# Kernel optimization log

Measured on AMD Instinct MI355X. Metric: run time of the kernel, lower is better.

The kernel has to match this reference:

```python
import jax, jax.numpy as jnp
import numpy as np

NUM_EXPERTS = 8
IN_FEATURES = 2048
OUT_FEATURES = 5632
GROUP_SIZE = 64
NUM_TOKENS = 4096


def setup_inputs() -> dict:
    key = jax.random.key(0)
    k1, k2, k3, k4 = jax.random.split(key, 4)
    inp = jax.random.normal(k1, (NUM_TOKENS, IN_FEATURES), dtype=jnp.float32)
    # tokens are pre-sorted contiguously per expert; balanced routing
    tokens_per_expert = jnp.full((NUM_EXPERTS,), NUM_TOKENS // NUM_EXPERTS, dtype=jnp.int32)
    # int4 quantized weights stored as integer codes in [0, 16)
    weights = jax.random.randint(k2, (NUM_EXPERTS, IN_FEATURES, OUT_FEATURES), 0, 16, dtype=jnp.int32)
    n_groups = IN_FEATURES // GROUP_SIZE
    scales = jax.random.uniform(k3, (NUM_EXPERTS, n_groups, OUT_FEATURES, 1), dtype=jnp.float32,
                                minval=0.005, maxval=0.02)
    zeros = jax.random.normal(k4, (NUM_EXPERTS, n_groups, OUT_FEATURES, 1), dtype=jnp.float32) * 0.01
    scales_and_zeros = jnp.concatenate([scales, zeros], axis=-1)  # [E, K//G, N, 2]
    return {"input": inp, "tokens_per_expert": tokens_per_expert,
            "weights": weights, "scales_and_zeros": scales_and_zeros}


def _dequant(weights, scales_and_zeros):
    # torchao int4 convention: w = (q - 8) * scale + zero, grouped along K
    E, K, N = weights.shape
    n_groups = scales_and_zeros.shape[1]
    g = K // n_groups
    q = weights.astype(jnp.float32).reshape(E, n_groups, g, N)
    s = scales_and_zeros[..., 0][:, :, None, :]  # [E, K//G, 1, N]
    z = scales_and_zeros[..., 1][:, :, None, :]
    return ((q - 8.0) * s + z).reshape(E, K, N)


def reference(input, tokens_per_expert, weights, scales_and_zeros):
    num_tokens, K = input.shape
    E = weights.shape[0]
    W = _dequant(weights, scales_and_zeros)  # [E, K, N] float32
    # expert id of each (contiguous-sorted) token from cumsum boundaries
    cum = jnp.cumsum(tokens_per_expert)                      # [E]
    seg = jnp.searchsorted(cum, jnp.arange(num_tokens), side='right')  # [T]
    start = jnp.concatenate([jnp.zeros((1,), cum.dtype), cum[:-1]])
    pos = jnp.arange(num_tokens) - start[seg]                # slot within expert block
    # capacity-based grouped GEMM (balanced routing in setup: C = T // E)
    C = num_tokens // E
    buf = jnp.zeros((E, C, K), input.dtype).at[seg, pos].set(input)
    y = jnp.einsum('eck,ekn->ecn', buf, W)                   # per-expert GEMM
    return y[seg, pos]                                       # [T, N]
```

## Files before the change

### kernel.cpp

```cpp
#include <hip/hip_runtime.h>

#define NE    8
#define KDIM  2048
#define NDIM  5632
#define NTOK  4096
#define CAP   512
#define NGRP  32
#define BM    128
#define BN    128
#define BK    32
#define MT    4
#define NT    44
#define LDSS  40

#define K8      (KDIM / 8)
#define NBLK_N  (NDIM / 256)
#define PACK_BLOCKS (NE * K8 * NBLK_N)
#define ACV_BLOCKS  (NTOK * KDIM / (8 * 256))
#define PACKED_BYTES ((size_t)NE * K8 * NDIM * 4)
#define ABF_BYTES    ((size_t)NTOK * KDIM * 2)
#define WBT_BYTES    ((size_t)NE * NDIM * KDIM * 2)

#define KB_DQ (KDIM / 64)
#define NB_DQ (NDIM / 256)
#define DQT_BLOCKS (NE * KB_DQ * NB_DQ)

typedef __attribute__((ext_vector_type(8))) short bf16x8;
typedef __attribute__((ext_vector_type(4))) short bf16x4;
typedef __attribute__((ext_vector_type(4))) float f32x4;

static __device__ __forceinline__ short f2bf(float f) {
    union { float f; unsigned u; } x; x.f = f;
    unsigned r = (x.u + 0x7fffu + ((x.u >> 16) & 1u)) >> 16;
    return (short)r;
}

static __device__ __forceinline__ void gl2lds16(const unsigned short* g, short* l) {
    __builtin_amdgcn_global_load_lds(
        (const __attribute__((address_space(1))) unsigned int*)g,
        (__attribute__((address_space(3))) unsigned int*)l, 16, 0, 0);
}

__global__ __launch_bounds__(256)
void dq_kernel(const int* __restrict__ wq, const float* __restrict__ sz,
               const float* __restrict__ inp,
               unsigned short* __restrict__ wbt, unsigned short* __restrict__ abf)
{
    const int bid = blockIdx.x;
    if (bid < DQT_BLOCKS) {
        const int e  = bid / (KB_DQ * NB_DQ);
        const int r  = bid % (KB_DQ * NB_DQ);
        const int kb = r / NB_DQ;
        const int nb = r % NB_DQ;
        const int n  = nb * 256 + threadIdx.x;

        const int* src = wq + ((size_t)e * KDIM + kb * 64) * NDIM + n;
        const float2 s2 = *(const float2*)(sz + (((size_t)e * NGRP + kb) * NDIM + n) * 2);
        const float s  = s2.x;
        const float z8 = s2.y - 8.f * s2.x;
        unsigned short* dst = wbt + ((size_t)e * NDIM + n) * KDIM + kb * 64;

        #pragma unroll
        for (int o = 0; o < 8; ++o) {
            bf16x8 h;
            #pragma unroll
            for (int j = 0; j < 8; ++j) {
                const float q = (float)src[(size_t)(o * 8 + j) * NDIM];
                h[j] = f2bf(fmaf(q, s, z8));
            }
            *(bf16x8*)(dst + o * 8) = h;
        }
    } else {
        const size_t t = (size_t)(bid - DQT_BLOCKS) * 256 + threadIdx.x;
        const float4* p = (const float4*)inp + t * 2;
        const float4 v0 = p[0], v1 = p[1];
        bf16x8 h;
        h[0] = f2bf(v0.x); h[1] = f2bf(v0.y); h[2] = f2bf(v0.z); h[3] = f2bf(v0.w);
        h[4] = f2bf(v1.x); h[5] = f2bf(v1.y); h[6] = f2bf(v1.z); h[7] = f2bf(v1.w);
        *((bf16x8*)abf + t) = h;
    }
}

__global__ __launch_bounds__(256)
void hqq_gemm3(const unsigned short* __restrict__ abf,
               const unsigned short* __restrict__ wbt,
               float* __restrict__ out)
{
    const int bid = blockIdx.x;
    const int e   = bid & 7;
    const int rem = bid >> 3;
    const int nt  = rem >> 2;
    const int mt  = rem & 3;

    __shared__ __align__(16) short Alds[BM * BK];
    __shared__ __align__(16) short Blds[BN * BK];

    const int tid = threadIdx.x;
    const int m0  = e * CAP + mt * BM;
    const int n0  = nt * BN;

    const unsigned short* Ab = abf + (size_t)m0 * KDIM;
    const unsigned short* Bb = wbt + ((size_t)e * NDIM + n0) * KDIM;

    f32x4 acc[4][4];
    #pragma unroll
    for (int i = 0; i < 4; ++i)
        #pragma unroll
        for (int j = 0; j < 4; ++j)
            acc[i][j] = (f32x4){0.f, 0.f, 0.f, 0.f};

    const int wave = tid >> 6;
    const int lane = tid & 63;
    const int wm = (wave >> 1) << 6;
    const int wn = (wave & 1) << 6;
    const int lr = lane & 15;
    const int lq = lane >> 4;

    for (int k0 = 0; k0 < KDIM; k0 += BK) {
        #pragma unroll
        for (int p = 0; p < 2; ++p) {
            const int idx = p * 256 + tid;
            const int row = idx >> 2;
            const int kq  = idx & 3;
            gl2lds16(Ab + (size_t)row * KDIM + k0 + kq * 8, &Alds[idx * 8]);
            gl2lds16(Bb + (size_t)row * KDIM + k0 + kq * 8, &Blds[idx * 8]);
        }
        __syncthreads();

        bf16x8 af[4], bv[4];
        #pragma unroll
        for (int i = 0; i < 4; ++i)
            af[i] = *(const bf16x8*)&Alds[(wm + i * 16 + lr) * BK + lq * 8];
        #pragma unroll
        for (int j = 0; j < 4; ++j)
            bv[j] = *(const bf16x8*)&Blds[(wn + j * 16 + lr) * BK + lq * 8];
        #pragma unroll
        for (int i = 0; i < 4; ++i)
            #pragma unroll
            for (int j = 0; j < 4; ++j)
                acc[i][j] = __builtin_amdgcn_mfma_f32_16x16x32_bf16(af[i], bv[j], acc[i][j], 0, 0, 0);

        __syncthreads();
    }

    const int orow0 = m0 + wm + lq * 4;
    const int ocol0 = n0 + wn + lr;
    #pragma unroll
    for (int i = 0; i < 4; ++i)
        #pragma unroll
        for (int r = 0; r < 4; ++r) {
            float* op = out + (size_t)(orow0 + i * 16 + r) * NDIM + ocol0;
            #pragma unroll
            for (int j = 0; j < 4; ++j)
                op[j * 16] = acc[i][j][r];
        }
}

__global__ __launch_bounds__(256)
void pack_kernel(const int* __restrict__ wq, const float* __restrict__ inp,
                 unsigned* __restrict__ pw, unsigned short* __restrict__ abf)
{
    const int bid = blockIdx.x;
    if (bid < PACK_BLOCKS) {
        const int e  = bid / (K8 * NBLK_N);
        const int r  = bid % (K8 * NBLK_N);
        const int k8 = r / NBLK_N;
        const int nb = r % NBLK_N;
        const int n  = nb * 256 + threadIdx.x;
        const int* src = wq + ((size_t)e * KDIM + k8 * 8) * NDIM + n;
        unsigned v = 0;
        #pragma unroll
        for (int j = 0; j < 8; ++j)
            v |= (unsigned)(src[(size_t)j * NDIM] & 15) << (4 * j);
        pw[((size_t)e * K8 + k8) * NDIM + n] = v;
    } else {
        const size_t t = (size_t)(bid - PACK_BLOCKS) * 256 + threadIdx.x;
        const float4* p = (const float4*)inp + t * 2;
        const float4 v0 = p[0], v1 = p[1];
        bf16x8 h;
        h[0] = f2bf(v0.x); h[1] = f2bf(v0.y); h[2] = f2bf(v0.z); h[3] = f2bf(v0.w);
        h[4] = f2bf(v1.x); h[5] = f2bf(v1.y); h[6] = f2bf(v1.z); h[7] = f2bf(v1.w);
        *((bf16x8*)abf + t) = h;
    }
}

__global__ __launch_bounds__(256, 2)
void hqq_gemm2(const unsigned short* __restrict__ abf,
               const unsigned*       __restrict__ pw,
               const float*          __restrict__ sz,
               float*                __restrict__ out)
{
    const int bid = blockIdx.x;
    const int e   = bid / (MT * NT);
    const int rem = bid % (MT * NT);
    const int nt  = rem >> 2;
    const int mt  = rem & 3;

    __shared__ __align__(16) short Alds[BM * LDSS];
    __shared__ __align__(16) short Blds[BN * LDSS];

    const int tid = threadIdx.x;
    const int m0  = e * CAP + mt * BM;
    const int n0  = nt * BN;

    const int a_kq  = tid & 3;
    const int a_row = tid >> 2;
    const int b_n   = tid & 127;
    const int b_h   = tid >> 7;

    const unsigned short* Ab = abf + (size_t)m0 * KDIM;
    const unsigned*       Wb = pw  + (size_t)e * K8 * NDIM + n0 + b_n;
    const float*          SZb = sz + (size_t)e * NGRP * (NDIM * 2) + (size_t)(n0 + b_n) * 2;

    f32x4 acc[4][4];
    #pragma unroll
    for (int i = 0; i < 4; ++i)
        #pragma unroll
        for (int j = 0; j < 4; ++j)
            acc[i][j] = (f32x4){0.f, 0.f, 0.f, 0.f};

    const int wave = tid >> 6;
    const int lane = tid & 63;
    const int wm = (wave >> 1) << 6;
    const int wn = (wave & 1) << 6;
    const int lr = lane & 15;
    const int lq = lane >> 4;

    for (int k0 = 0; k0 < KDIM; k0 += BK) {
        const int g = k0 >> 6;
        #pragma unroll
        for (int p = 0; p < 2; ++p) {
            const int row = a_row + p * 64;
            const bf16x8 v = *(const bf16x8*)(Ab + (size_t)row * KDIM + k0 + a_kq * 8);
            *(bf16x8*)&Alds[row * LDSS + a_kq * 8] = v;
        }
        const float2 s2 = *(const float2*)(SZb + (size_t)g * (NDIM * 2));
        const float s  = s2.x;
        const float z8 = s2.y - 8.f * s2.x;
        const unsigned* wp = Wb + ((size_t)(k0 >> 3) + b_h * 2) * NDIM;
        const unsigned u0 = wp[0];
        const unsigned u1 = wp[NDIM];
        bf16x8 bb0, bb1;
        #pragma unroll
        for (int j = 0; j < 8; ++j) {
            bb0[j] = f2bf(fmaf((float)((u0 >> (4 * j)) & 15u), s, z8));
            bb1[j] = f2bf(fmaf((float)((u1 >> (4 * j)) & 15u), s, z8));
        }
        *(bf16x8*)&Blds[b_n * LDSS + b_h * 16]     = bb0;
        *(bf16x8*)&Blds[b_n * LDSS + b_h * 16 + 8] = bb1;

        __syncthreads();

        bf16x8 af[4], bfv[4];
        #pragma unroll
        for (int i = 0; i < 4; ++i)
            af[i] = *(const bf16x8*)&Alds[(wm + i * 16 + lr) * LDSS + lq * 8];
        #pragma unroll
        for (int j = 0; j < 4; ++j)
            bfv[j] = *(const bf16x8*)&Blds[(wn + j * 16 + lr) * LDSS + lq * 8];
        #pragma unroll
        for (int i = 0; i < 4; ++i)
            #pragma unroll
            for (int j = 0; j < 4; ++j)
                acc[i][j] = __builtin_amdgcn_mfma_f32_16x16x32_bf16(af[i], bfv[j], acc[i][j], 0, 0, 0);

        __syncthreads();
    }

    const int orow0 = m0 + wm + lq * 4;
    const int ocol0 = n0 + wn + lr;
    #pragma unroll
    for (int i = 0; i < 4; ++i)
        #pragma unroll
        for (int r = 0; r < 4; ++r) {
            float* op = out + (size_t)(orow0 + i * 16 + r) * NDIM + ocol0;
            #pragma unroll
            for (int j = 0; j < 4; ++j)
                op[j * 16] = acc[i][j][r];
        }
}

__global__ __launch_bounds__(256, 2)
void hqq_gemm_fallback(const float* __restrict__ inp,
                       const int*   __restrict__ wq,
                       const float* __restrict__ sz,
                       float*       __restrict__ out)
{
    const int bid = blockIdx.x;
    const int e   = bid / (MT * NT);
    const int rem = bid % (MT * NT);
    const int nt  = rem >> 2;
    const int mt  = rem & 3;

    __shared__ __align__(16) short Alds[BM * LDSS];
    __shared__ __align__(16) short Blds[BN * LDSS];

    const int tid = threadIdx.x;
    const int m0  = e * CAP + mt * BM;
    const int n0  = nt * BN;

    const int a_kq  = tid & 7;
    const int a_row = tid >> 3;
    const int b_n   = tid & 127;
    const int b_h   = tid >> 7;

    const float* Ab  = inp + (size_t)m0 * KDIM;
    const int*   Wb  = wq  + (size_t)e * KDIM * NDIM + n0 + b_n;
    const float* SZb = sz  + (size_t)e * NGRP * (NDIM * 2) + (size_t)(n0 + b_n) * 2;

    f32x4 acc[4][4];
    #pragma unroll
    for (int i = 0; i < 4; ++i)
        #pragma unroll
        for (int j = 0; j < 4; ++j)
            acc[i][j] = (f32x4){0.f, 0.f, 0.f, 0.f};

    const int wave = tid >> 6;
    const int lane = tid & 63;
    const int wm = (wave >> 1) << 6;
    const int wn = (wave & 1) << 6;
    const int lr = lane & 15;
    const int lq = lane >> 4;

    for (int k0 = 0; k0 < KDIM; k0 += BK) {
        const int g = k0 >> 6;
        #pragma unroll
        for (int p = 0; p < 4; ++p) {
            const int row = a_row + p * 32;
            const float4 v = *(const float4*)(Ab + (size_t)row * KDIM + k0 + a_kq * 4);
            bf16x4 h;
            h[0] = f2bf(v.x); h[1] = f2bf(v.y); h[2] = f2bf(v.z); h[3] = f2bf(v.w);
            *(bf16x4*)&Alds[row * LDSS + a_kq * 4] = h;
        }
        const float2 s2 = *(const float2*)(SZb + (size_t)g * (NDIM * 2));
        const float s  = s2.x;
        const float z8 = s2.y - 8.f * s2.x;
        #pragma unroll
        for (int oo = 0; oo < 2; ++oo) {
            const int ko = b_h * 8 + oo * 16;
            const int* wp = Wb + (size_t)(k0 + ko) * NDIM;
            bf16x8 bb;
            #pragma unroll
            for (int j = 0; j < 8; ++j) {
                const float q = (float)wp[(size_t)j * NDIM];
                bb[j] = f2bf(fmaf(q, s, z8));
            }
            *(bf16x8*)&Blds[b_n * LDSS + ko] = bb;
        }
        __syncthreads();
        bf16x8 af[4], bfv[4];
        #pragma unroll
        for (int i = 0; i < 4; ++i)
            af[i] = *(const bf16x8*)&Alds[(wm + i * 16 + lr) * LDSS + lq * 8];
        #pragma unroll
        for (int j = 0; j < 4; ++j)
            bfv[j] = *(const bf16x8*)&Blds[(wn + j * 16 + lr) * LDSS + lq * 8];
        #pragma unroll
        for (int i = 0; i < 4; ++i)
            #pragma unroll
            for (int j = 0; j < 4; ++j)
                acc[i][j] = __builtin_amdgcn_mfma_f32_16x16x32_bf16(af[i], bfv[j], acc[i][j], 0, 0, 0);
        __syncthreads();
    }

    const int orow0 = m0 + wm + lq * 4;
    const int ocol0 = n0 + wn + lr;
    #pragma unroll
    for (int i = 0; i < 4; ++i)
        #pragma unroll
        for (int r = 0; r < 4; ++r) {
            float* op = out + (size_t)(orow0 + i * 16 + r) * NDIM + ocol0;
            #pragma unroll
            for (int j = 0; j < 4; ++j)
                op[j * 16] = acc[i][j][r];
        }
}

extern "C" void kernel_launch(void* const* d_in, const int* in_sizes, int n_in,
                              void* d_out, int out_size, void* d_ws, size_t ws_size,
                              hipStream_t stream) {
    const float* inp = (const float*)d_in[0];
    const int*   wq  = (const int*)d_in[2];
    const float* sz  = (const float*)d_in[3];
    float*       out = (float*)d_out;

    if (ws_size >= ABF_BYTES + WBT_BYTES) {
        unsigned short* abf = (unsigned short*)d_ws;
        unsigned short* wbt = (unsigned short*)((char*)d_ws + ABF_BYTES);
        dq_kernel<<<dim3(DQT_BLOCKS + ACV_BLOCKS), dim3(256), 0, stream>>>(wq, sz, inp, wbt, abf);
        hqq_gemm3<<<dim3(NE * MT * NT), dim3(256), 0, stream>>>(abf, wbt, out);
    } else if (ws_size >= PACKED_BYTES + ABF_BYTES) {
        unsigned*       pw  = (unsigned*)d_ws;
        unsigned short* abf = (unsigned short*)((char*)d_ws + PACKED_BYTES);
        pack_kernel<<<dim3(PACK_BLOCKS + ACV_BLOCKS), dim3(256), 0, stream>>>(wq, inp, pw, abf);
        hqq_gemm2<<<dim3(NE * MT * NT), dim3(256), 0, stream>>>(abf, pw, sz, out);
    } else {
        hqq_gemm_fallback<<<dim3(NE * MT * NT), dim3(256), 0, stream>>>(inp, wq, sz, out);
    }
}
```

Baseline: 831.7 us.

## Transpose dequantized weights through swizzled LDS tiles for coalesced loads and stores

Each dequant-transpose block now handles a 128x128 (K,N) tile. It reads int32 codes with vectorized int4 loads, writes bf16 values into an XOR-swizzled shared-memory tile, and after a barrier writes contiguous 16-byte chunks along K into the transposed weight buffer. Before this, each thread walked a strided column and stored 16 bytes per row, which gave poorly coalesced global writes. In exchange the change uses 32 KB of LDS per block and adds a barrier, which can reduce occupancy for this pre-pass.

```diff
diff --git a/kernel.cpp b/kernel.cpp
--- a/kernel.cpp
+++ b/kernel.cpp
@@ -21,9 +21,9 @@
 #define ABF_BYTES    ((size_t)NTOK * KDIM * 2)
 #define WBT_BYTES    ((size_t)NE * NDIM * KDIM * 2)
 
-#define KB_DQ (KDIM / 64)
-#define NB_DQ (NDIM / 256)
-#define DQT_BLOCKS (NE * KB_DQ * NB_DQ)
+#define KT_DQ (KDIM / 128)
+#define NT_DQ (NDIM / 128)
+#define DQT_BLOCKS (NE * KT_DQ * NT_DQ)
 
 typedef __attribute__((ext_vector_type(8))) short bf16x8;
 typedef __attribute__((ext_vector_type(4))) short bf16x4;
@@ -48,27 +48,71 @@
 {
     const int bid = blockIdx.x;
     if (bid < DQT_BLOCKS) {
-        const int e  = bid / (KB_DQ * NB_DQ);
-        const int r  = bid % (KB_DQ * NB_DQ);
-        const int kb = r / NB_DQ;
-        const int nb = r % NB_DQ;
-        const int n  = nb * 256 + threadIdx.x;
-
-        const int* src = wq + ((size_t)e * KDIM + kb * 64) * NDIM + n;
-        const float2 s2 = *(const float2*)(sz + (((size_t)e * NGRP + kb) * NDIM + n) * 2);
-        const float s  = s2.x;
-        const float z8 = s2.y - 8.f * s2.x;
-        unsigned short* dst = wbt + ((size_t)e * NDIM + n) * KDIM + kb * 64;
-
-        #pragma unroll
-        for (int o = 0; o < 8; ++o) {
-            bf16x8 h;
-            #pragma unroll
-            for (int j = 0; j < 8; ++j) {
-                const float q = (float)src[(size_t)(o * 8 + j) * NDIM];
-                h[j] = f2bf(fmaf(q, s, z8));
+        const int e  = bid / (KT_DQ * NT_DQ);
+        const int r  = bid % (KT_DQ * NT_DQ);
+        const int kt = r / NT_DQ;
+        const int ntb = r % NT_DQ;
+        const int k0 = kt * 128;
+        const int n0 = ntb * 128;
+        const int t  = threadIdx.x;
+
+        __shared__ __align__(16) short T[128 * 128];
+
+        const int col  = t & 31;
+        const int band = t >> 5;
+        const int g    = (k0 >> 6) + (band >> 2);
+
+        float s_[4], z_[4];
+        #pragma unroll
+        for (int j = 0; j < 4; ++j) {
+            const int n = n0 + col * 4 + j;
+            const float2 s2 = *(const float2*)(sz + (((size_t)e * NGRP + g) * NDIM + n) * 2);
+            s_[j] = s2.x;
+            z_[j] = s2.y - 8.f * s2.x;
+        }
+
+        const int* src = wq + ((size_t)e * KDIM + k0 + band * 16) * NDIM + n0 + col * 4;
+
+        #pragma unroll
+        for (int p4 = 0; p4 < 4; ++p4) {
+            int4 v0 = *(const int4*)(src + (size_t)(p4 * 4 + 0) * NDIM);
+            int4 v1 = *(const int4*)(src + (size_t)(p4 * 4 + 1) * NDIM);
+            int4 v2 = *(const int4*)(src + (size_t)(p4 * 4 + 2) * NDIM);
+            int4 v3 = *(const int4*)(src + (size_t)(p4 * 4 + 3) * NDIM);
+            const int kb = band * 16 + p4 * 4;
+            const int slotbase = kb >> 3;
+            const int halfoff  = (kb & 7);
+
+            #pragma unroll
+            for (int j = 0; j < 4; ++j) {
+                const int q0 = (j == 0) ? v0.x : (j == 1) ? v0.y : (j == 2) ? v0.z : v0.w;
+                const int q1 = (j == 0) ? v1.x : (j == 1) ? v1.y : (j == 2) ? v1.z : v1.w;
+                const int q2 = (j == 0) ? v2.x : (j == 1) ? v2.y : (j == 2) ? v2.z : v2.w;
+                const int q3 = (j == 0) ? v3.x : (j == 1) ? v3.y : (j == 2) ? v3.z : v3.w;
+                bf16x4 quad;
+                quad[0] = f2bf(fmaf((float)q0, s_[j], z_[j]));
+                quad[1] = f2bf(fmaf((float)q1, s_[j], z_[j]));
+                quad[2] = f2bf(fmaf((float)q2, s_[j], z_[j]));
+                quad[3] = f2bf(fmaf((float)q3, s_[j], z_[j]));
+                const int n_l = col * 4 + j;
+                const int addr = n_l * 128 + ((slotbase ^ (n_l & 15)) << 3) + halfoff;
+                *(bf16x4*)&T[addr] = quad;
             }
-            *(bf16x8*)(dst + o * 8) = h;
+        }
+
+        __syncthreads();
+
+        const int wc = t & 7;
+        const int wn = t >> 3;
+        #pragma unroll
+        for (int p = 0; p < 4; ++p) {
+            const int n_l = wn + p * 32;
+            const int x = n_l & 15;
+            unsigned short* dst = wbt + ((size_t)e * NDIM + n0 + n_l) * KDIM + k0;
+            const bf16x8 r0 = *(const bf16x8*)&T[n_l * 128 + ((wc ^ x) << 3)];
+            const bf16x8 r1 = *(const bf16x8*)&T[n_l * 128 + (((wc + 8) ^ x) << 3)];
+            *(bf16x8*)(dst + wc * 8) = r0;
+            *(bf16x8*)(dst + (wc + 8) * 8) = r1;
         }
     } else {
         const size_t t = (size_t)(bid - DQT_BLOCKS) * 256 + threadIdx.x;
```

Measured after the change: 738.1 us. 11.2% less time.
